# Kernel tuning notes

Hardware: AMD Instinct MI355X
Metric: run time of the kernel (lower is better)

## Reference

```python
import jax, jax.numpy as jnp
import numpy as np

N = 4096
K = 3          # from loss_name 'LMNN-3'
MU = 0.5       # default mu in LMNN
NUM_CLASSES = 10


def setup_inputs() -> dict:
    key = jax.random.key(0)
    k1, k2 = jax.random.split(key)
    distances_sq = jax.random.uniform(k1, (N, N), dtype=jnp.float32)
    labels = jax.random.randint(k2, (N, 1), 0, NUM_CLASSES, dtype=jnp.int32)
    return {"distances_sq": distances_sq, "labels": labels}


def lmnn(D, labels, k=K, mu=MU):
    n = D.shape[0]
    same = (labels == labels.T).astype(D.dtype)              # [n,n] same-class indicator
    cross = same * (1.0 - jnp.eye(n, dtype=D.dtype))         # exclude self-pairs
    order = jnp.argsort(D, axis=-1)                          # ascending per row
    pull_mask = jnp.take_along_axis(cross, order, axis=-1)[:, : k + 1]   # [n,k+1]
    sortD = jnp.take_along_axis(D, order, axis=-1)[:, : k + 1]           # [n,k+1]
    pull_d = sortD * pull_mask                               # masked k+1 nearest distances
    pull = jnp.sum(pull_d)
    # push: sum_{i,m,j} relu((pull_d[i,m] - D[j,i] + 1) * pull_mask[i,m] * (1 - same[j,i]))
    # vectorized form of the original per-row Python loop; hinge is [n, k+1, n]
    hinge = jax.nn.relu(
        (pull_d[:, :, None] - D.T[:, None, :] + 1.0)
        * pull_mask[:, :, None]
        * (1.0 - same.T)[:, None, :]
    )
    push = jnp.sum(hinge)
    return (1.0 - mu) * pull + mu * push


def reference(distances_sq, labels):
    # grad_reverse is identity in the forward pass
    return lmnn(distances_sq, labels)
```

## Files before the change

kernel.cpp:

```cpp
#include <hip/hip_runtime.h>

#define N 4096
#define NCLS 10
#define RPB 16
#define NCHUNK (N / RPB)
#define NSLICE 4
#define CAPS 64
#define THRESH 0.015625f
#define CRG 8
#define CRC (NCHUNK / CRG)

__device__ __forceinline__ bool lessvi(float v1, int i1, float v2, int i2) {
    return (v1 < v2) || (v1 == v2 && i1 < i2);
}

__device__ __forceinline__ void insert4(float vv, int ci, float tv[4], int ti[4]) {
    if (lessvi(vv, ci, tv[3], ti[3])) {
        tv[3] = vv; ti[3] = ci;
#pragma unroll
        for (int q2 = 3; q2 > 0; --q2) {
            const bool sw = lessvi(tv[q2], ti[q2], tv[q2 - 1], ti[q2 - 1]);
            const float av = tv[q2 - 1]; const int ai = ti[q2 - 1];
            tv[q2 - 1] = sw ? tv[q2] : av;
            ti[q2 - 1] = sw ? ti[q2] : ai;
            tv[q2]     = sw ? av : tv[q2];
            ti[q2]     = sw ? ai : ti[q2];
        }
    }
}

__global__ __launch_bounds__(256) void stream2d(const float* __restrict__ D,
                                                const int* __restrict__ labels,
                                                float* __restrict__ pdiff,
                                                float* __restrict__ cand_v,
                                                int* __restrict__ cand_i,
                                                int* __restrict__ cand_cnt) {
    __shared__ int scnt[RPB];
    const int tid   = threadIdx.x;
    const int slice = blockIdx.x & 3;
    const int chunk = blockIdx.x >> 2;
    const int r0    = chunk * RPB;
    const int c0    = slice * 1024 + tid * 4;

    if (tid < RPB) scnt[tid] = 0;
    __syncthreads();

    const int4 cl = *(const int4*)(labels + c0);
    float4 diff = {0.f, 0.f, 0.f, 0.f};

    const float* rowbase = D + (size_t)r0 * N + slice * 1024;
    float4 vc = ((const float4*)rowbase)[tid];

#pragma unroll
    for (int r = 0; r < RPB; ++r) {
        float4 vn;
        if (r < RPB - 1) vn = ((const float4*)(rowbase + (size_t)(r + 1) * N))[tid];
        const int row    = r0 + r;
        const int rowlab = labels[row];

        diff.x += (cl.x != rowlab) ? vc.x : 0.f;
        diff.y += (cl.y != rowlab) ? vc.y : 0.f;
        diff.z += (cl.z != rowlab) ? vc.z : 0.f;
        diff.w += (cl.w != rowlab) ? vc.w : 0.f;

        const float vals[4] = {vc.x, vc.y, vc.z, vc.w};
#pragma unroll
        for (int e = 0; e < 4; ++e) {
            if (vals[e] < THRESH) {
                const int idx = atomicAdd(&scnt[r], 1);
                if (idx < CAPS) {
                    const size_t slot = (size_t)row * (NSLICE * CAPS) + slice * CAPS + idx;
                    cand_v[slot] = vals[e];
                    cand_i[slot] = c0 + e;
                }
            }
        }
        vc = vn;
    }

    *(float4*)(pdiff + (size_t)chunk * N + c0) = diff;

    __syncthreads();
    if (tid < RPB) cand_cnt[(size_t)(r0 + tid) * NSLICE + slice] = scnt[tid];
}

__global__ __launch_bounds__(256) void select_top4(const float* __restrict__ D,
                                                   const int* __restrict__ labels,
                                                   const float* __restrict__ cand_v,
                                                   const int* __restrict__ cand_i,
                                                   const int* __restrict__ cand_cnt,
                                                   float* __restrict__ pd_sum,
                                                   float* __restrict__ a_cnt) {
    const int lane = threadIdx.x & 63;
    const int wave = threadIdx.x >> 6;
    const int row  = blockIdx.x * 4 + wave;

    const int4 cnt4 = *(const int4*)(cand_cnt + (size_t)row * NSLICE);
    const int cs[4] = {cnt4.x, cnt4.y, cnt4.z, cnt4.w};
    const int total = cs[0] + cs[1] + cs[2] + cs[3];
    const bool ok = (total >= 4) && (cs[0] <= CAPS) && (cs[1] <= CAPS) &&
                    (cs[2] <= CAPS) && (cs[3] <= CAPS);

    float tv[4] = {INFINITY, INFINITY, INFINITY, INFINITY};
    int   ti[4] = {0x7ffffff0, 0x7ffffff1, 0x7ffffff2, 0x7ffffff3};

    if (ok) {
#pragma unroll
        for (int s = 0; s < 4; ++s) {
            const size_t base = (size_t)row * (NSLICE * CAPS) + s * CAPS;
            for (int k = lane; k < cs[s]; k += 64)
                insert4(cand_v[base + k], cand_i[base + k], tv, ti);
        }
    } else {
        const float4* rp4 = (const float4*)(D + (size_t)row * N);
        for (int s = 0; s < 16; ++s) {
            const float4 q = rp4[s * 64 + lane];
            const int cc = (s * 64 + lane) * 4;
            insert4(q.x, cc, tv, ti);
            insert4(q.y, cc + 1, tv, ti);
            insert4(q.z, cc + 2, tv, ti);
            insert4(q.w, cc + 3, tv, ti);
        }
    }

#pragma unroll
    for (int off = 1; off < 64; off <<= 1) {
        float yv[4]; int yi[4];
#pragma unroll
        for (int k = 0; k < 4; ++k) {
            yv[k] = __shfl_xor(tv[k], off);
            yi[k] = __shfl_xor(ti[k], off);
        }
        float rv[4]; int ri[4];
#pragma unroll
        for (int k = 0; k < 4; ++k) {
            const bool tm = lessvi(tv[0], ti[0], yv[0], yi[0]);
            rv[k] = tm ? tv[0] : yv[0];
            ri[k] = tm ? ti[0] : yi[0];
#pragma unroll
            for (int q2 = 0; q2 < 3; ++q2) {
                tv[q2] = tm ? tv[q2 + 1] : tv[q2];
                ti[q2] = tm ? ti[q2 + 1] : ti[q2];
                yv[q2] = tm ? yv[q2]     : yv[q2 + 1];
                yi[q2] = tm ? yi[q2]     : yi[q2 + 1];
            }
        }
#pragma unroll
        for (int k = 0; k < 4; ++k) { tv[k] = rv[k]; ti[k] = ri[k]; }
    }

    if (lane == 0) {
        const int li = labels[row];
        float pd = 0.f, a = 0.f;
#pragma unroll
        for (int m = 0; m < 4; ++m) {
            const int j = ti[m];
            if (j != row && labels[j] == li) { pd += tv[m]; a += 1.f; }
        }
        pd_sum[row] = pd;
        a_cnt[row]  = a;
    }
}

__global__ __launch_bounds__(256) void col_reduce(const float* __restrict__ pdiff,
                                                  float* __restrict__ cdiff) {
    const int tile = blockIdx.x & 3;
    const int g    = blockIdx.x >> 2;
    const int col  = tile * 1024 + threadIdx.x * 4;
    float4 acc = {0.f, 0.f, 0.f, 0.f};
#pragma unroll 8
    for (int ch = 0; ch < CRC; ++ch) {
        const float4 v = *(const float4*)(pdiff + (size_t)(g * CRC + ch) * N + col);
        acc.x += v.x; acc.y += v.y; acc.z += v.z; acc.w += v.w;
    }
    *(float4*)(cdiff + (size_t)g * N + col) = acc;
}

__global__ __launch_bounds__(256) void finalize(const int* __restrict__ labels,
                                                const float* __restrict__ pd_sum,
                                                const float* __restrict__ a_cnt,
                                                const float* __restrict__ cdiff,
                                                float* __restrict__ out) {
    __shared__ int    cnt[NCLS];
    __shared__ double red[256];
    const int tid = threadIdx.x;

    if (tid < NCLS) cnt[tid] = 0;
    __syncthreads();
    for (int i = tid; i < N; i += 256) atomicAdd(&cnt[labels[i]], 1);
    __syncthreads();

    double acc = 0.0;
    for (int i = tid; i < N; i += 256) {
        const int li = labels[i];
        const double pd = (double)pd_sum[i];
        const double a  = (double)a_cnt[i];
        float csf = 0.f;
#pragma unroll
        for (int g = 0; g < CRG; ++g) csf += cdiff[(size_t)g * N + i];
        const double cs = (double)csf;
        const double cd = (double)(N - cnt[li]);
        acc += pd;
        acc += cd * (pd + a) - a * cs;
    }
    red[tid] = acc;
    __syncthreads();
    for (int s = 128; s > 0; s >>= 1) {
        if (tid < s) red[tid] += red[tid + s];
        __syncthreads();
    }
    if (tid == 0) out[0] = (float)(0.5 * red[0]);
}

extern "C" void kernel_launch(void* const* d_in, const int* in_sizes, int n_in,
                              void* d_out, int out_size, void* d_ws, size_t ws_size,
                              hipStream_t stream) {
    const float* D      = (const float*)d_in[0];
    const int*   labels = (const int*)d_in[1];
    float*       out    = (float*)d_out;

    float* pdiff    = (float*)d_ws;
    float* cdiff    = pdiff + (size_t)NCHUNK * N;
    float* pd_sum   = cdiff + (size_t)CRG * N;
    float* a_cnt    = pd_sum + N;
    float* cand_v   = a_cnt + N;
    int*   cand_i   = (int*)(cand_v + (size_t)N * NSLICE * CAPS);
    int*   cand_cnt = cand_i + (size_t)N * NSLICE * CAPS;

    stream2d<<<NCHUNK * NSLICE, 256, 0, stream>>>(D, labels, pdiff, cand_v, cand_i, cand_cnt);
    select_top4<<<N / 4, 256, 0, stream>>>(D, labels, cand_v, cand_i, cand_cnt, pd_sum, a_cnt);
    col_reduce<<<CRG * 4, 256, 0, stream>>>(pdiff, cdiff);
    finalize<<<1, 256, 0, stream>>>(labels, pd_sum, a_cnt, cdiff, out);
}
```

Baseline: 121.6 us.

## Stage candidates in LDS, widen stream slices, fuse column reduce into select

The streaming kernel now covers 2048 columns per block (two float4 per thread) with a 3-deep register prefetch, so it launches half as many blocks. Threshold candidates go to shared memory first and are written out coalesced per row at the end, instead of as scattered global stores. The column-reduce kernel is merged into the top-4 select launch as extra blocks, which removes one kernel launch. The trade-off is fewer blocks for the streaming pass, more registers per thread, and a per-row-per-slice candidate cap that now covers twice as many columns, so the fallback full-row scan may trigger more often.

```diff
diff --git a/kernel.cpp b/kernel.cpp
--- a/kernel.cpp
+++ b/kernel.cpp
@@ -4,11 +4,13 @@
 #define NCLS 10
 #define RPB 16
 #define NCHUNK (N / RPB)
-#define NSLICE 4
+#define NSLICE 2
 #define CAPS 64
 #define THRESH 0.015625f
 #define CRG 8
 #define CRC (NCHUNK / CRG)
+#define SELBLK (N / 4)
+#define FOLDBLK (CRG * 4)
 
 __device__ __forceinline__ bool lessvi(float v1, int i1, float v2, int i2) {
     return (v1 < v2) || (v1 == v2 && i1 < i2);
@@ -35,78 +37,124 @@
                                                 float* __restrict__ cand_v,
                                                 int* __restrict__ cand_i,
                                                 int* __restrict__ cand_cnt) {
-    __shared__ int scnt[RPB];
+    __shared__ int   scnt[RPB];
+    __shared__ float lv[RPB][CAPS];
+    __shared__ int   li[RPB][CAPS];
+
     const int tid   = threadIdx.x;
-    const int slice = blockIdx.x & 3;
-    const int chunk = blockIdx.x >> 2;
+    const int lane  = tid & 63;
+    const int wave  = tid >> 6;
+    const int slice = blockIdx.x & (NSLICE - 1);
+    const int chunk = blockIdx.x >> 1;
     const int r0    = chunk * RPB;
-    const int c0    = slice * 1024 + tid * 4;
+    const int c0    = slice * 2048 + tid * 4;
+    const int c1    = c0 + 1024;
 
     if (tid < RPB) scnt[tid] = 0;
     __syncthreads();
 
-    const int4 cl = *(const int4*)(labels + c0);
-    float4 diff = {0.f, 0.f, 0.f, 0.f};
-
-    const float* rowbase = D + (size_t)r0 * N + slice * 1024;
-    float4 vc = ((const float4*)rowbase)[tid];
+    const int4 clA = *(const int4*)(labels + c0);
+    const int4 clB = *(const int4*)(labels + c1);
+    float4 dA = {0.f, 0.f, 0.f, 0.f};
+    float4 dB = {0.f, 0.f, 0.f, 0.f};
+
+    const float4* rb = (const float4*)(D + (size_t)r0 * N + slice * 2048);
+    float4 bufA[3], bufB[3];
+    bufA[0] = rb[tid];        bufB[0] = rb[tid + 256];
+    bufA[1] = rb[1024 + tid]; bufB[1] = rb[1024 + tid + 256];
 
 #pragma unroll
     for (int r = 0; r < RPB; ++r) {
-        float4 vn;
-        if (r < RPB - 1) vn = ((const float4*)(rowbase + (size_t)(r + 1) * N))[tid];
-        const int row    = r0 + r;
-        const int rowlab = labels[row];
-
-        diff.x += (cl.x != rowlab) ? vc.x : 0.f;
-        diff.y += (cl.y != rowlab) ? vc.y : 0.f;
-        diff.z += (cl.z != rowlab) ? vc.z : 0.f;
-        diff.w += (cl.w != rowlab) ? vc.w : 0.f;
-
-        const float vals[4] = {vc.x, vc.y, vc.z, vc.w};
+        if (r + 2 < RPB) {
+            bufA[(r + 2) % 3] = rb[(size_t)(r + 2) * 1024 + tid];
+            bufB[(r + 2) % 3] = rb[(size_t)(r + 2) * 1024 + tid + 256];
+        }
+        const float4 cA = bufA[r % 3];
+        const float4 cB = bufB[r % 3];
+        const int rowlab = labels[r0 + r];
+
+        dA.x += (clA.x != rowlab) ? cA.x : 0.f;
+        dA.y += (clA.y != rowlab) ? cA.y : 0.f;
+        dA.z += (clA.z != rowlab) ? cA.z : 0.f;
+        dA.w += (clA.w != rowlab) ? cA.w : 0.f;
+        dB.x += (clB.x != rowlab) ? cB.x : 0.f;
+        dB.y += (clB.y != rowlab) ? cB.y : 0.f;
+        dB.z += (clB.z != rowlab) ? cB.z : 0.f;
+        dB.w += (clB.w != rowlab) ? cB.w : 0.f;
+
+        const float va[4] = {cA.x, cA.y, cA.z, cA.w};
+        const float vb[4] = {cB.x, cB.y, cB.z, cB.w};
 #pragma unroll
         for (int e = 0; e < 4; ++e) {
-            if (vals[e] < THRESH) {
+            if (va[e] < THRESH) {
                 const int idx = atomicAdd(&scnt[r], 1);
-                if (idx < CAPS) {
-                    const size_t slot = (size_t)row * (NSLICE * CAPS) + slice * CAPS + idx;
-                    cand_v[slot] = vals[e];
-                    cand_i[slot] = c0 + e;
-                }
+                if (idx < CAPS) { lv[r][idx] = va[e]; li[r][idx] = c0 + e; }
             }
         }
-        vc = vn;
-    }
-
-    *(float4*)(pdiff + (size_t)chunk * N + c0) = diff;
-
-    __syncthreads();
-    if (tid < RPB) cand_cnt[(size_t)(r0 + tid) * NSLICE + slice] = scnt[tid];
-}
-
-__global__ __launch_bounds__(256) void select_top4(const float* __restrict__ D,
+#pragma unroll
+        for (int e = 0; e < 4; ++e) {
+            if (vb[e] < THRESH) {
+                const int idx = atomicAdd(&scnt[r], 1);
+                if (idx < CAPS) { lv[r][idx] = vb[e]; li[r][idx] = c1 + e; }
+            }
+        }
+    }
+
+    *(float4*)(pdiff + (size_t)chunk * N + c0) = dA;
+    *(float4*)(pdiff + (size_t)chunk * N + c1) = dB;
+
+    __syncthreads();
+    for (int rr = wave; rr < RPB; rr += 4) {
+        const int c   = scnt[rr];
+        const int row = r0 + rr;
+        if (lane == 0) cand_cnt[(size_t)row * NSLICE + slice] = c;
+        if (lane < (c < CAPS ? c : CAPS)) {
+            const size_t slot = (size_t)row * (NSLICE * CAPS) + slice * CAPS + lane;
+            cand_v[slot] = lv[rr][lane];
+            cand_i[slot] = li[rr][lane];
+        }
+    }
+}
+
+__global__ __launch_bounds__(256) void select_fold(const float* __restrict__ D,
                                                    const int* __restrict__ labels,
                                                    const float* __restrict__ cand_v,
                                                    const int* __restrict__ cand_i,
                                                    const int* __restrict__ cand_cnt,
+                                                   const float* __restrict__ pdiff,
                                                    float* __restrict__ pd_sum,
-                                                   float* __restrict__ a_cnt) {
+                                                   float* __restrict__ a_cnt,
+                                                   float* __restrict__ cdiff) {
+    if (blockIdx.x >= SELBLK) {
+        const int fb   = blockIdx.x - SELBLK;
+        const int tile = fb & 3;
+        const int g    = fb >> 2;
+        const int col  = tile * 1024 + threadIdx.x * 4;
+        float4 acc = {0.f, 0.f, 0.f, 0.f};
+#pragma unroll 8
+        for (int ch = 0; ch < CRC; ++ch) {
+            const float4 v = *(const float4*)(pdiff + (size_t)(g * CRC + ch) * N + col);
+            acc.x += v.x; acc.y += v.y; acc.z += v.z; acc.w += v.w;
+        }
+        *(float4*)(cdiff + (size_t)g * N + col) = acc;
+        return;
+    }
+
     const int lane = threadIdx.x & 63;
     const int wave = threadIdx.x >> 6;
     const int row  = blockIdx.x * 4 + wave;
 
-    const int4 cnt4 = *(const int4*)(cand_cnt + (size_t)row * NSLICE);
-    const int cs[4] = {cnt4.x, cnt4.y, cnt4.z, cnt4.w};
-    const int total = cs[0] + cs[1] + cs[2] + cs[3];
-    const bool ok = (total >= 4) && (cs[0] <= CAPS) && (cs[1] <= CAPS) &&
-                    (cs[2] <= CAPS) && (cs[3] <= CAPS);
+    const int2 cnt2 = *(const int2*)(cand_cnt + (size_t)row * NSLICE);
+    const int total = cnt2.x + cnt2.y;
+    const bool ok = (total >= 4) && (cnt2.x <= CAPS) && (cnt2.y <= CAPS);
 
     float tv[4] = {INFINITY, INFINITY, INFINITY, INFINITY};
     int   ti[4] = {0x7ffffff0, 0x7ffffff1, 0x7ffffff2, 0x7ffffff3};
 
     if (ok) {
-#pragma unroll
-        for (int s = 0; s < 4; ++s) {
+        const int cs[2] = {cnt2.x, cnt2.y};
+#pragma unroll
+        for (int s = 0; s < 2; ++s) {
             const size_t base = (size_t)row * (NSLICE * CAPS) + s * CAPS;
             for (int k = lane; k < cs[s]; k += 64)
                 insert4(cand_v[base + k], cand_i[base + k], tv, ti);
@@ -150,30 +198,16 @@
     }
 
     if (lane == 0) {
-        const int li = labels[row];
+        const int li2 = labels[row];
         float pd = 0.f, a = 0.f;
 #pragma unroll
         for (int m = 0; m < 4; ++m) {
             const int j = ti[m];
-            if (j != row && labels[j] == li) { pd += tv[m]; a += 1.f; }
+            if (j != row && labels[j] == li2) { pd += tv[m]; a += 1.f; }
         }
         pd_sum[row] = pd;
         a_cnt[row]  = a;
     }
-}
-
-__global__ __launch_bounds__(256) void col_reduce(const float* __restrict__ pdiff,
-                                                  float* __restrict__ cdiff) {
-    const int tile = blockIdx.x & 3;
-    const int g    = blockIdx.x >> 2;
-    const int col  = tile * 1024 + threadIdx.x * 4;
-    float4 acc = {0.f, 0.f, 0.f, 0.f};
-#pragma unroll 8
-    for (int ch = 0; ch < CRC; ++ch) {
-        const float4 v = *(const float4*)(pdiff + (size_t)(g * CRC + ch) * N + col);
-        acc.x += v.x; acc.y += v.y; acc.z += v.z; acc.w += v.w;
-    }
-    *(float4*)(cdiff + (size_t)g * N + col) = acc;
 }
 
 __global__ __launch_bounds__(256) void finalize(const int* __restrict__ labels,
@@ -228,7 +262,7 @@
     int*   cand_cnt = cand_i + (size_t)N * NSLICE * CAPS;
 
     stream2d<<<NCHUNK * NSLICE, 256, 0, stream>>>(D, labels, pdiff, cand_v, cand_i, cand_cnt);
-    select_top4<<<N / 4, 256, 0, stream>>>(D, labels, cand_v, cand_i, cand_cnt, pd_sum, a_cnt);
-    col_reduce<<<CRG * 4, 256, 0, stream>>>(pdiff, cdiff);
+    select_fold<<<SELBLK + FOLDBLK, 256, 0, stream>>>(D, labels, cand_v, cand_i, cand_cnt,
+                                                      pdiff, pd_sum, a_cnt, cdiff);
     finalize<<<1, 256, 0, stream>>>(labels, pd_sum, a_cnt, cdiff, out);
 }
```

Result: faster. 110.9 us (-8.7%).
